# Performance work log

Measured on AMD Instinct MI355X. Metric: run time of the kernel, lower is better.

Reference implementation:

```python
import jax, jax.numpy as jnp
import numpy as np

D_MODEL = 64
D_K = 64
D_V = 64
SEQ = 8192
MASK_VAL = 10.0 ** 10  # matches original: scores - 1e10 * triu_mask


def setup_inputs() -> dict:
    key = jax.random.key(0)
    ks = jax.random.split(key, 7)
    s = 1.0 / np.sqrt(D_MODEL)
    return {
        "x": jax.random.normal(ks[0], (SEQ, D_MODEL), dtype=jnp.float32),
        "w_q": jax.random.uniform(ks[1], (D_K, D_MODEL), jnp.float32, -s, s),
        "b_q": jax.random.uniform(ks[2], (D_K,), jnp.float32, -s, s),
        "w_k": jax.random.uniform(ks[3], (D_K, D_MODEL), jnp.float32, -s, s),
        "b_k": jax.random.uniform(ks[4], (D_K,), jnp.float32, -s, s),
        "w_v": jax.random.uniform(ks[5], (D_V, D_MODEL), jnp.float32, -s, s),
        "b_v": jax.random.uniform(ks[6], (D_V,), jnp.float32, -s, s),
    }


def reference(x, w_q, b_q, w_k, b_k, w_v, b_v):
    # torch Linear: y = x @ W.T + b
    q = x @ w_q.T + b_q            # [S, d_k]
    k = x @ w_k.T + b_k            # [S, d_k]
    v = x @ w_v.T + b_v            # [S, d_v]
    scores = (q @ k.T) / jnp.sqrt(jnp.float32(D_K))  # [S, S]
    S = scores.shape[0]
    # upper-triangular (strict) causal mask, subtracted with large constant
    mask = jnp.triu(jnp.ones((S, S), dtype=scores.dtype), k=1)
    attn = jax.nn.softmax(scores - MASK_VAL * mask, axis=1)
    return attn @ v                # [S, d_v]
```

## Files before the change

### kernel.cpp

```cpp
#include <hip/hip_runtime.h>

#define SEQ 8192
#define DM 64

typedef __bf16 bfrag __attribute__((ext_vector_type(8)));
typedef __bf16 b4v   __attribute__((ext_vector_type(4)));
typedef float  f4    __attribute__((ext_vector_type(4)));

union PW { int w[4]; bfrag v; };

#define QSCALE 0.1803368801111204f

#define GLOAD16(gsrc, ldst)                                                \
    __builtin_amdgcn_global_load_lds(                                      \
        (const __attribute__((address_space(1))) unsigned int*)(gsrc),     \
        (__attribute__((address_space(3))) unsigned int*)(ldst), 16, 0, 0)

__device__ inline float fexp2(float x) {
    float y;
    asm("v_exp_f32 %0, %1" : "=v"(y) : "v"(x));
    return y;
}

__device__ inline int pack_bf16(float a, float b) {
    const __bf16 ba = (__bf16)a, bb = (__bf16)b;
    const unsigned short ua = __builtin_bit_cast(unsigned short, ba);
    const unsigned short ub = __builtin_bit_cast(unsigned short, bb);
    return (int)(((unsigned)ub << 16) | (unsigned)ua);
}

__device__ inline void split8(const float* __restrict__ p, bfrag& hi, bfrag& lo) {
    #pragma unroll
    for (int e = 0; e < 8; ++e) {
        const float v = p[e];
        const __bf16 h = (__bf16)v;
        hi[e] = h;
        lo[e] = (__bf16)(v - (float)h);
    }
}

__global__ __launch_bounds__(256) void qkv_proj(
    const float* __restrict__ x,
    const float* __restrict__ wq, const float* __restrict__ bq,
    const float* __restrict__ wk, const float* __restrict__ bk,
    const float* __restrict__ wv, const float* __restrict__ bv,
    __bf16* __restrict__ Qb, __bf16* __restrict__ Ks, __bf16* __restrict__ Vg)
{
    const int lane = threadIdx.x & 63;
    const int wid  = threadIdx.x >> 6;
    const int task = blockIdx.x * 4 + wid;
    const int m    = task >> 11;
    const int rest = task & 2047;
    const int rt   = rest >> 2;
    const int dt   = rest & 3;
    const int rb   = rt << 4;
    const int g = lane >> 4, r = lane & 15;

    const float* w = (m == 0) ? wq : (m == 1) ? wk : wv;

    bfrag xhi[2], xlo[2];
    #pragma unroll
    for (int kh = 0; kh < 2; ++kh)
        split8(x + (rb + r) * DM + kh * 32 + g * 8, xhi[kh], xlo[kh]);
    bfrag whi[2], wlo[2];
    #pragma unroll
    for (int kh = 0; kh < 2; ++kh)
        split8(w + (dt * 16 + r) * DM + kh * 32 + g * 8, whi[kh], wlo[kh]);

    if (m < 2) {
        f4 acc = {0.f, 0.f, 0.f, 0.f};
        #pragma unroll
        for (int kh = 0; kh < 2; ++kh) {
            acc = __builtin_amdgcn_mfma_f32_16x16x32_bf16(whi[kh], xhi[kh], acc, 0, 0, 0);
            acc = __builtin_amdgcn_mfma_f32_16x16x32_bf16(wlo[kh], xhi[kh], acc, 0, 0, 0);
            acc = __builtin_amdgcn_mfma_f32_16x16x32_bf16(whi[kh], xlo[kh], acc, 0, 0, 0);
        }
        const float* bias = (m == 0) ? bq : bk;
        const int c0 = dt * 16 + g * 4;
        const float4 b4 = *(const float4*)(bias + c0);
        const float sc = (m == 0) ? QSCALE : 1.0f;
        b4v pv;
        pv[0] = (__bf16)((acc[0] + b4.x) * sc);
        pv[1] = (__bf16)((acc[1] + b4.y) * sc);
        pv[2] = (__bf16)((acc[2] + b4.z) * sc);
        pv[3] = (__bf16)((acc[3] + b4.w) * sc);
        if (m == 0) {
            *(b4v*)(Qb + (rb + r) * DM + c0) = pv;
        } else {
            const int row = rb + r, t = row >> 5, row32 = row & 31;
            const int ch  = dt * 2 + (g >> 1);
            const int b2  = ((row32 >> 4) << 1) | (ch >> 2);
            *(b4v*)(Ks + t * 2048 + b2 * 512 + (ch & 3) * 128
                       + (row32 & 15) * 8 + (g & 1) * 4) = pv;
        }
    } else {
        f4 acc = {0.f, 0.f, 0.f, 0.f};
        #pragma unroll
        for (int kh = 0; kh < 2; ++kh) {
            acc = __builtin_amdgcn_mfma_f32_16x16x32_bf16(xhi[kh], whi[kh], acc, 0, 0, 0);
            acc = __builtin_amdgcn_mfma_f32_16x16x32_bf16(xlo[kh], whi[kh], acc, 0, 0, 0);
            acc = __builtin_amdgcn_mfma_f32_16x16x32_bf16(xhi[kh], wlo[kh], acc, 0, 0, 0);
        }
        const int d  = dt * 16 + r;
        const float bd = bv[d];
        const int L0 = (rb & 31) + g * 4;
        const int P0 = ((L0 & 15) >> 2) * 8 + (L0 >> 4) * 4;
        const int t  = rb >> 5;
        b4v pv;
        pv[0] = (__bf16)(acc[0] + bd);
        pv[1] = (__bf16)(acc[1] + bd);
        pv[2] = (__bf16)(acc[2] + bd);
        pv[3] = (__bf16)(acc[3] + bd);
        *(b4v*)(Vg + t * 2048 + (d >> 4) * 512 + (P0 >> 3) * 128
                   + (d & 15) * 8 + (P0 & 7)) = pv;
    }
}

__global__ __launch_bounds__(256)
__attribute__((amdgpu_waves_per_eu(4)))
void flash_attn(
    const __bf16* __restrict__ Qb, const __bf16* __restrict__ Ks,
    const __bf16* __restrict__ Vg,
    float* __restrict__ Opart, float* __restrict__ Lpart)
{
    __shared__ __align__(16) unsigned char smem[34816];

    const int tid  = threadIdx.x;
    const int lane = tid & 63;
    const int wid  = tid >> 6;
    const int b    = blockIdx.x;
    const int fam  = b >> 2;
    const int g4   = b & 3;
    const int grp  = fam >> 6, hh = fam & 63;
    const int qt   = (grp == 0) ? (255 - hh) : (grp == 1) ? hh
                   : (grp == 2) ? (191 - hh) : (64 + hh);
    const int qbase = qt * 32;
    const int gq = lane >> 4;
    const int r  = lane & 15;
    const int lo16 = lane << 4;

    bfrag qf[2][2];
    #pragma unroll
    for (int sub = 0; sub < 2; ++sub)
        #pragma unroll
        for (int kh = 0; kh < 2; ++kh)
            qf[sub][kh] = *(const bfrag*)(Qb + (qbase + sub * 16 + r) * DM + kh * 32 + gq * 8);

    f4 o[2][4] = {};
    float ls[2] = {0.f, 0.f};

    const int ntiles = qt + 1;
    const int f0 = g4 * 4;
    const int nsteps = (ntiles > f0) ? ((ntiles - f0 + 15) >> 4) : 0;

    const char* Kbb = (const char*)Ks;
    const char* Vbb = (const char*)Vg;

    auto stage = [&](int s, int buf) {
        const int base = (f0 + s * 16) * 4096;
        #pragma unroll
        for (int jr = 0; jr < 4; ++jr) {
            const int st = jr * 4 + wid;
            GLOAD16(Kbb + base + st * 1024 + lo16, smem + buf * 16384 + st * 1024);
        }
    };

    int cur = 0;
    if (nsteps > 0) stage(0, 0);
    __syncthreads();

    for (int s = 0; s < nsteps; ++s) {
        const int j = f0 + s * 16 + wid;
        bfrag vf[4];
        #pragma unroll
        for (int dt = 0; dt < 4; ++dt)
            vf[dt] = *(const bfrag*)(Vbb + j * 4096 + dt * 1024 + lo16);
        if (s + 1 < nsteps) stage(s + 1, cur ^ 1);

        const unsigned char* Kr = smem + cur * 16384 + wid * 4096;
        const bfrag kf0 = *(const bfrag*)(Kr + lo16);
        const bfrag kf1 = *(const bfrag*)(Kr + 1024 + lo16);
        const bfrag kf2 = *(const bfrag*)(Kr + 2048 + lo16);
        const bfrag kf3 = *(const bfrag*)(Kr + 3072 + lo16);

        const int kvb = j * 32 + gq * 4;
        #pragma unroll
        for (int sub = 0; sub < 2; ++sub) {
            f4 sh0 = {}, sh1 = {};
            sh0 = __builtin_amdgcn_mfma_f32_16x16x32_bf16(kf0, qf[sub][0], sh0, 0, 0, 0);
            sh0 = __builtin_amdgcn_mfma_f32_16x16x32_bf16(kf1, qf[sub][1], sh0, 0, 0, 0);
            sh1 = __builtin_amdgcn_mfma_f32_16x16x32_bf16(kf2, qf[sub][0], sh1, 0, 0, 0);
            sh1 = __builtin_amdgcn_mfma_f32_16x16x32_bf16(kf3, qf[sub][1], sh1, 0, 0, 0);

            const int qg = qbase + sub * 16 + r;
            float p0[4], p1[4];
            #pragma unroll
            for (int e = 0; e < 4; ++e) {
                p0[e] = (kvb + e      <= qg) ? fexp2(sh0[e]) : 0.f;
                p1[e] = (kvb + e + 16 <= qg) ? fexp2(sh1[e]) : 0.f;
            }
            ls[sub] += (p0[0] + p0[1]) + (p0[2] + p0[3])
                     + (p1[0] + p1[1]) + (p1[2] + p1[3]);

            PW pu;
            pu.w[0] = pack_bf16(p0[0], p0[1]); pu.w[1] = pack_bf16(p0[2], p0[3]);
            pu.w[2] = pack_bf16(p1[0], p1[1]); pu.w[3] = pack_bf16(p1[2], p1[3]);

            #pragma unroll
            for (int dt = 0; dt < 4; ++dt)
                o[sub][dt] = __builtin_amdgcn_mfma_f32_16x16x32_bf16(pu.v, vf[dt], o[sub][dt], 0, 0, 0);
        }

        __syncthreads();
        cur ^= 1;
    }

    float* Ol  = (float*)smem;
    float* Lsm = (float*)(smem + 33792);
    #pragma unroll
    for (int sub = 0; sub < 2; ++sub) {
        ls[sub] += __shfl_xor(ls[sub], 16, 64);
        ls[sub] += __shfl_xor(ls[sub], 32, 64);
        if (lane < 16) Lsm[wid * 32 + sub * 16 + r] = ls[sub];
        #pragma unroll
        for (int dt = 0; dt < 4; ++dt)
            #pragma unroll
            for (int e = 0; e < 4; ++e)
                Ol[(wid * 32 + sub * 16 + gq * 4 + e) * 66 + dt * 16 + r] = o[sub][dt][e];
    }
    __syncthreads();

    for (int i = tid; i < 32 * 64; i += 256) {
        const int row = i >> 6, col = i & 63;
        const float sum = Ol[(row) * 66 + col] + Ol[(32 + row) * 66 + col]
                        + Ol[(64 + row) * 66 + col] + Ol[(96 + row) * 66 + col];
        Opart[((long long)g4 * SEQ + qbase + row) * DM + col] = sum;
    }
    if (tid < 32) {
        const float l = Lsm[tid] + Lsm[32 + tid] + Lsm[64 + tid] + Lsm[96 + tid];
        Lpart[g4 * SEQ + qbase + tid] = l;
    }
}

__global__ __launch_bounds__(256) void normalize(
    const float* __restrict__ Opart, const float* __restrict__ Lpart,
    float* __restrict__ out)
{
    const int i = blockIdx.x * 256 + threadIdx.x;
    const f4* O = (const f4*)Opart;
    const int N = SEQ * DM / 4;
    const int row = i >> 4;
    const f4 a0 = O[i], a1 = O[N + i], a2 = O[2 * N + i], a3 = O[3 * N + i];
    const float l = (Lpart[row] + Lpart[SEQ + row])
                  + (Lpart[2 * SEQ + row] + Lpart[3 * SEQ + row]);
    const float inv = 1.0f / l;
    f4 res;
    #pragma unroll
    for (int e = 0; e < 4; ++e) res[e] = ((a0[e] + a1[e]) + (a2[e] + a3[e])) * inv;
    ((f4*)out)[i] = res;
}

extern "C" void kernel_launch(void* const* d_in, const int* in_sizes, int n_in,
                              void* d_out, int out_size, void* d_ws, size_t ws_size,
                              hipStream_t stream)
{
    (void)in_sizes; (void)n_in; (void)out_size; (void)ws_size;
    const float* x  = (const float*)d_in[0];
    const float* wq = (const float*)d_in[1];
    const float* bq = (const float*)d_in[2];
    const float* wk = (const float*)d_in[3];
    const float* bk = (const float*)d_in[4];
    const float* wv = (const float*)d_in[5];
    const float* bv = (const float*)d_in[6];
    float* out = (float*)d_out;

    __bf16* Qb = (__bf16*)d_ws;
    __bf16* Ks = Qb + SEQ * DM;
    __bf16* Vg = Ks + SEQ * DM;
    float*  Opart = (float*)(Vg + SEQ * DM);
    float*  Lpart = Opart + 4 * SEQ * DM;

    qkv_proj<<<1536, 256, 0, stream>>>(x, wq, bq, wk, bk, wv, bv, Qb, Ks, Vg);
    flash_attn<<<1024, 256, 0, stream>>>(Qb, Ks, Vg, Opart, Lpart);
    normalize<<<SEQ * DM / 4 / 256, 256, 0, stream>>>(Opart, Lpart, out);
}
```

Measured before the change: 37.20 us.

## Skip dead KV tiles, unmask interior tiles, compute row sums via MFMA

Waves whose KV tile lies beyond the causal diagonal now skip the V loads and all MFMA/exp work. Tiles strictly below the diagonal drop the per-element mask comparisons. Row sums of P are accumulated by an extra MFMA against a ones vector instead of scalar adds plus shuffles, so the sums now come from the bf16-rounded P, which matches what multiplies V. bf16 packing uses the hardware v_cvt_pk_bf16_f32 instruction.

```diff
diff --git a/kernel.cpp b/kernel.cpp
--- a/kernel.cpp
+++ b/kernel.cpp
@@ -22,11 +22,10 @@
     return y;
 }
 
-__device__ inline int pack_bf16(float a, float b) {
-    const __bf16 ba = (__bf16)a, bb = (__bf16)b;
-    const unsigned short ua = __builtin_bit_cast(unsigned short, ba);
-    const unsigned short ub = __builtin_bit_cast(unsigned short, bb);
-    return (int)(((unsigned)ub << 16) | (unsigned)ua);
+__device__ inline int cvtpk(float a, float b) {
+    int d;
+    asm("v_cvt_pk_bf16_f32 %0, %1, %2" : "=v"(d) : "v"(a), "v"(b));
+    return d;
 }
 
 __device__ inline void split8(const float* __restrict__ p, bfrag& hi, bfrag& lo) {
@@ -146,8 +145,12 @@
         for (int kh = 0; kh < 2; ++kh)
             qf[sub][kh] = *(const bfrag*)(Qb + (qbase + sub * 16 + r) * DM + kh * 32 + gq * 8);
 
+    bfrag ones;
+    #pragma unroll
+    for (int e = 0; e < 8; ++e) ones[e] = (__bf16)1.0f;
+
     f4 o[2][4] = {};
-    float ls[2] = {0.f, 0.f};
+    f4 lsacc[2] = {};
 
     const int ntiles = qt + 1;
     const int f0 = g4 * 4;
@@ -171,44 +174,56 @@
 
     for (int s = 0; s < nsteps; ++s) {
         const int j = f0 + s * 16 + wid;
+        const bool live = (j <= qt);
         bfrag vf[4];
-        #pragma unroll
-        for (int dt = 0; dt < 4; ++dt)
-            vf[dt] = *(const bfrag*)(Vbb + j * 4096 + dt * 1024 + lo16);
-        if (s + 1 < nsteps) stage(s + 1, cur ^ 1);
-
-        const unsigned char* Kr = smem + cur * 16384 + wid * 4096;
-        const bfrag kf0 = *(const bfrag*)(Kr + lo16);
-        const bfrag kf1 = *(const bfrag*)(Kr + 1024 + lo16);
-        const bfrag kf2 = *(const bfrag*)(Kr + 2048 + lo16);
-        const bfrag kf3 = *(const bfrag*)(Kr + 3072 + lo16);
-
-        const int kvb = j * 32 + gq * 4;
-        #pragma unroll
-        for (int sub = 0; sub < 2; ++sub) {
-            f4 sh0 = {}, sh1 = {};
-            sh0 = __builtin_amdgcn_mfma_f32_16x16x32_bf16(kf0, qf[sub][0], sh0, 0, 0, 0);
-            sh0 = __builtin_amdgcn_mfma_f32_16x16x32_bf16(kf1, qf[sub][1], sh0, 0, 0, 0);
-            sh1 = __builtin_amdgcn_mfma_f32_16x16x32_bf16(kf2, qf[sub][0], sh1, 0, 0, 0);
-            sh1 = __builtin_amdgcn_mfma_f32_16x16x32_bf16(kf3, qf[sub][1], sh1, 0, 0, 0);
-
-            const int qg = qbase + sub * 16 + r;
-            float p0[4], p1[4];
-            #pragma unroll
-            for (int e = 0; e < 4; ++e) {
-                p0[e] = (kvb + e      <= qg) ? fexp2(sh0[e]) : 0.f;
-                p1[e] = (kvb + e + 16 <= qg) ? fexp2(sh1[e]) : 0.f;
-            }
-            ls[sub] += (p0[0] + p0[1]) + (p0[2] + p0[3])
-                     + (p1[0] + p1[1]) + (p1[2] + p1[3]);
-
-            PW pu;
-            pu.w[0] = pack_bf16(p0[0], p0[1]); pu.w[1] = pack_bf16(p0[2], p0[3]);
-            pu.w[2] = pack_bf16(p1[0], p1[1]); pu.w[3] = pack_bf16(p1[2], p1[3]);
-
+        if (live) {
             #pragma unroll
             for (int dt = 0; dt < 4; ++dt)
-                o[sub][dt] = __builtin_amdgcn_mfma_f32_16x16x32_bf16(pu.v, vf[dt], o[sub][dt], 0, 0, 0);
+                vf[dt] = *(const bfrag*)(Vbb + j * 4096 + dt * 1024 + lo16);
+        }
+        if (s + 1 < nsteps) stage(s + 1, cur ^ 1);
+
+        if (live) {
+            const unsigned char* Kr = smem + cur * 16384 + wid * 4096;
+            const bfrag kf0 = *(const bfrag*)(Kr + lo16);
+            const bfrag kf1 = *(const bfrag*)(Kr + 1024 + lo16);
+            const bfrag kf2 = *(const bfrag*)(Kr + 2048 + lo16);
+            const bfrag kf3 = *(const bfrag*)(Kr + 3072 + lo16);
+
+            const int kvb = j * 32 + gq * 4;
+            #pragma unroll
+            for (int sub = 0; sub < 2; ++sub) {
+                f4 sh0 = {}, sh1 = {};
+                sh0 = __builtin_amdgcn_mfma_f32_16x16x32_bf16(kf0, qf[sub][0], sh0, 0, 0, 0);
+                sh0 = __builtin_amdgcn_mfma_f32_16x16x32_bf16(kf1, qf[sub][1], sh0, 0, 0, 0);
+                sh1 = __builtin_amdgcn_mfma_f32_16x16x32_bf16(kf2, qf[sub][0], sh1, 0, 0, 0);
+                sh1 = __builtin_amdgcn_mfma_f32_16x16x32_bf16(kf3, qf[sub][1], sh1, 0, 0, 0);
+
+                float p0[4], p1[4];
+                if (j < qt) {
+                    #pragma unroll
+                    for (int e = 0; e < 4; ++e) {
+                        p0[e] = fexp2(sh0[e]);
+                        p1[e] = fexp2(sh1[e]);
+                    }
+                } else {
+                    const int qg = qbase + sub * 16 + r;
+                    #pragma unroll
+                    for (int e = 0; e < 4; ++e) {
+                        p0[e] = (kvb + e      <= qg) ? fexp2(sh0[e]) : 0.f;
+                        p1[e] = (kvb + e + 16 <= qg) ? fexp2(sh1[e]) : 0.f;
+                    }
+                }
+
+                PW pu;
+                pu.w[0] = cvtpk(p0[0], p0[1]); pu.w[1] = cvtpk(p0[2], p0[3]);
+                pu.w[2] = cvtpk(p1[0], p1[1]); pu.w[3] = cvtpk(p1[2], p1[3]);
+
+                lsacc[sub] = __builtin_amdgcn_mfma_f32_16x16x32_bf16(pu.v, ones, lsacc[sub], 0, 0, 0);
+                #pragma unroll
+                for (int dt = 0; dt < 4; ++dt)
+                    o[sub][dt] = __builtin_amdgcn_mfma_f32_16x16x32_bf16(pu.v, vf[dt], o[sub][dt], 0, 0, 0);
+            }
         }
 
         __syncthreads();
@@ -219,9 +234,10 @@
     float* Lsm = (float*)(smem + 33792);
     #pragma unroll
     for (int sub = 0; sub < 2; ++sub) {
-        ls[sub] += __shfl_xor(ls[sub], 16, 64);
-        ls[sub] += __shfl_xor(ls[sub], 32, 64);
-        if (lane < 16) Lsm[wid * 32 + sub * 16 + r] = ls[sub];
+        if (r == 0)
+            #pragma unroll
+            for (int e = 0; e < 4; ++e)
+                Lsm[wid * 32 + sub * 16 + gq * 4 + e] = lsacc[sub][e];
         #pragma unroll
         for (int dt = 0; dt < 4; ++dt)
             #pragma unroll
```

Result: faster. 35.76 us (-3.8%).
